# Performance work log

Measured on AMD Instinct MI355X. Metric: run time of the kernel, lower is better.

The kernel has to match this reference:

```python
import jax, jax.numpy as jnp
import numpy as np

N_STATE = 1024
N_HEAD = 16
DIM_PER_HEAD = N_STATE // N_HEAD  # 64
QK_SCALE = DIM_PER_HEAD ** (-0.5)
B, T, T_CACHE = 8, 256, 768


def setup_inputs() -> dict:
    key = jax.random.key(0)
    ks = jax.random.split(key, 12)
    s = 0.02
    return {
        "x": jax.random.normal(ks[0], (B, T, N_STATE), dtype=jnp.float32),
        "qk_mask": jnp.zeros((T, T_CACHE + T), dtype=jnp.float32),
        "cache_k": jax.random.normal(ks[1], (B, T_CACHE, N_STATE), dtype=jnp.float32),
        "cache_v": jax.random.normal(ks[2], (B, T_CACHE, N_STATE), dtype=jnp.float32),
        "Wq": jax.random.normal(ks[3], (N_STATE, N_STATE), dtype=jnp.float32) * s,
        "bq": jax.random.normal(ks[4], (N_STATE,), dtype=jnp.float32) * s,
        "Wk": jax.random.normal(ks[5], (N_STATE, N_STATE), dtype=jnp.float32) * s,
        "Wv": jax.random.normal(ks[6], (N_STATE, N_STATE), dtype=jnp.float32) * s,
        "bv": jax.random.normal(ks[7], (N_STATE,), dtype=jnp.float32) * s,
        "Wo": jax.random.normal(ks[8], (N_STATE, N_STATE), dtype=jnp.float32) * s,
        "bo": jax.random.normal(ks[9], (N_STATE,), dtype=jnp.float32) * s,
    }


def reference(x, qk_mask, cache_k, cache_v, Wq, bq, Wk, Wv, bv, Wo, bo):
    # Linear projections (weights stored as [in, out], i.e. torch weight^T)
    q = (x @ Wq + bq) * QK_SCALE            # [B, T, D]
    new_k = x @ Wk                           # key has no bias
    new_v = x @ Wv + bv
    # KV-cache concat along time
    k = jnp.concatenate([cache_k, new_k], axis=1)  # [B, Tkv, D]
    v = jnp.concatenate([cache_v, new_v], axis=1)
    # Split heads
    Bq, Tq = q.shape[:2]
    Tkv = k.shape[1]
    qh = q.reshape(Bq, Tq, N_HEAD, DIM_PER_HEAD)    # [B, T, H, d]
    kh = k.reshape(Bq, Tkv, N_HEAD, DIM_PER_HEAD)
    vh = v.reshape(Bq, Tkv, N_HEAD, DIM_PER_HEAD)
    # q @ k^T + mask, softmax over keys
    qk = jnp.einsum("bthd,bshd->bhts", qh, kh) + qk_mask  # [B, H, T, Tkv]
    w = jax.nn.softmax(qk, axis=-1).astype(qh.dtype)
    wv = jnp.einsum("bhts,bshd->bthd", w, vh).reshape(Bq, Tq, N_STATE)
    out = wv @ Wo + bo
    return out, new_k, new_v
```

## Files before the change

kernel.cpp:

```cpp
#include <hip/hip_runtime.h>
#include <hip/hip_bf16.h>
#include <stdint.h>

#define Bb 8
#define Tt 256
#define TCC 768
#define TKV 1024
#define NS 1024
#define NH 16
#define DH 64
#define QK_SCALE 0.125f

typedef short bf16x8 __attribute__((ext_vector_type(8)));
typedef float f32x4 __attribute__((ext_vector_type(4)));
typedef unsigned int u32;

__device__ __forceinline__ unsigned short f2bf(float f) {
  union { float f; uint32_t u; } v; v.f = f;
  uint32_t u = v.u;
  u += 0x7fff + ((u >> 16) & 1);
  return (unsigned short)(u >> 16);
}

__device__ __forceinline__ void gload16(const unsigned short* g, unsigned short* l) {
  __builtin_amdgcn_global_load_lds(
      (__attribute__((address_space(1))) u32*)g,
      (__attribute__((address_space(3))) u32*)l,
      16, 0, 0);
}

__global__ __launch_bounds__(256) void prep(
    const float* __restrict__ x, const float* __restrict__ ck,
    const float* __restrict__ Wq, const float* __restrict__ Wk,
    const float* __restrict__ Wv, const float* __restrict__ Wo,
    const float* __restrict__ cv,
    unsigned short* __restrict__ xb, unsigned short* __restrict__ kbw,
    unsigned short* __restrict__ wqt, unsigned short* __restrict__ wkt,
    unsigned short* __restrict__ wvt, unsigned short* __restrict__ wot,
    unsigned short* __restrict__ vbt) {
  __shared__ float tile[64][65];
  int bid = blockIdx.x, tid = threadIdx.x;
  if (bid < 2048) {
    const int64_t nx4 = (int64_t)Bb * Tt * NS / 4;
    const int64_t nk4 = (int64_t)Bb * TCC * NS / 4;
    const int64_t stride = 2048LL * 256;
    for (int64_t t = (int64_t)bid * 256 + tid; t < nx4 + nk4; t += stride) {
      if (t < nx4) {
        float4 v = ((const float4*)x)[t];
        ushort4 o; o.x = f2bf(v.x); o.y = f2bf(v.y); o.z = f2bf(v.z); o.w = f2bf(v.w);
        ((ushort4*)xb)[t] = o;
      } else {
        int64_t e = t - nx4;
        float4 v = ((const float4*)ck)[e];
        ushort4 o; o.x = f2bf(v.x); o.y = f2bf(v.y); o.z = f2bf(v.z); o.w = f2bf(v.w);
        int64_t el = e * 4;
        int64_t b = el / ((int64_t)TCC * NS);
        int64_t rem = el % ((int64_t)TCC * NS);
        int64_t d = b * (int64_t)TKV * NS + rem;
        ((ushort4*)kbw)[d / 4] = o;
      }
    }
    return;
  }
  int tb = bid - 2048;
  const float* src; unsigned short* dst;
  if (tb < 1024) {
    int mat = tb >> 8, t = tb & 255;
    int tr = t >> 4, tc = t & 15;
    const float* W = (mat == 0) ? Wq : (mat == 1) ? Wk : (mat == 2) ? Wv : Wo;
    unsigned short* Wt = (mat == 0) ? wqt : (mat == 1) ? wkt : (mat == 2) ? wvt : wot;
    src = W + (int64_t)(tr * 64) * 1024 + tc * 64;
    dst = Wt + (int64_t)(tc * 64) * 1024 + tr * 64;
  } else {
    int e = tb - 1024;
    int b = e / 192; int t = e % 192;
    int st = t >> 4, ct = t & 15;
    src = cv + (int64_t)b * TCC * NS + (int64_t)(st * 64) * 1024 + ct * 64;
    dst = vbt + (int64_t)b * NS * TKV + (int64_t)(ct * 64) * 1024 + st * 64;
  }
  for (int e = tid; e < 1024; e += 256) {
    int i = e >> 4, j4 = (e & 15) * 4;
    float4 v = *(const float4*)&src[(int64_t)i * 1024 + j4];
    tile[i][j4] = v.x; tile[i][j4 + 1] = v.y; tile[i][j4 + 2] = v.z; tile[i][j4 + 3] = v.w;
  }
  __syncthreads();
  for (int e = tid; e < 1024; e += 256) {
    int i = e >> 4, j4 = (e & 15) * 4;
    ushort4 o;
    o.x = f2bf(tile[j4][i]); o.y = f2bf(tile[j4 + 1][i]);
    o.z = f2bf(tile[j4 + 2][i]); o.w = f2bf(tile[j4 + 3][i]);
    *(ushort4*)&dst[(int64_t)i * 1024 + j4] = o;
  }
}

template <int MODE>
__global__ __launch_bounds__(256) void gemm_mfma(
    const unsigned short* __restrict__ A,
    const unsigned short* __restrict__ Bt0, const unsigned short* __restrict__ Bt1,
    const unsigned short* __restrict__ Bt2,
    const float* __restrict__ bq, const float* __restrict__ bv,
    const float* __restrict__ bo,
    unsigned short* __restrict__ qb,
    float* __restrict__ okf, float* __restrict__ ovf,
    unsigned short* __restrict__ kb, unsigned short* __restrict__ vbt,
    float* __restrict__ outf) {
  constexpr int BM = 64;
  constexpr int BN = (MODE == 0) ? 128 : 64;
  constexpr int MT = 2;
  constexpr int NTf = BN / 32;
  __shared__ __align__(16) unsigned short As[2][BM * 64];
  __shared__ __align__(16) unsigned short Bs[2][BN * 64];

  int tid = threadIdx.x, lane = tid & 63, w = tid >> 6;
  int lr = lane & 15, hi = lane >> 4;
  int wm = w >> 1, wn = w & 1;

  int bid = blockIdx.x;
  int cpx = gridDim.x >> 3;
  int logical = (bid & 7) * cpx + (bid >> 3);

  int tm = logical & 31;
  int tn = logical >> 5;
  int seg, col0;
  const unsigned short* Bt;
  if (MODE == 0) {
    seg = tn >> 3; col0 = (tn & 7) * 128;
    Bt = (seg == 0) ? Bt0 : (seg == 1) ? Bt1 : Bt2;
  } else {
    seg = 0; col0 = tn * 64;
    Bt = Bt0;
  }
  int m0 = tm * 64;

  int srow = lane >> 3;
  int sch8 = (((lane & 7) ^ srow)) * 8;
  int sw = lr & 7;

  f32x4 acc[MT][NTf];
#pragma unroll
  for (int i = 0; i < MT; i++)
#pragma unroll
    for (int j = 0; j < NTf; j++) acc[i][j] = (f32x4){0.f, 0.f, 0.f, 0.f};

  auto STAGE = [&](int buf, int k0) {
#pragma unroll
    for (int i = 0; i < 2; i++) {
      int rb = w * 16 + i * 8;
      gload16(&A[(int64_t)(m0 + rb + srow) * 1024 + k0 + sch8], &As[buf][rb * 64]);
    }
#pragma unroll
    for (int i = 0; i < BN / 32; i++) {
      int rb = w * (BN / 4) + i * 8;
      gload16(&Bt[(int64_t)(col0 + rb + srow) * 1024 + k0 + sch8], &Bs[buf][rb * 64]);
    }
  };

  STAGE(0, 0);
  __syncthreads();
  int cur = 0;
  for (int step = 0; step < 16; ++step) {
    if (step < 15) STAGE(cur ^ 1, (step + 1) * 64);
    bf16x8 af[2][MT], bfr[2][NTf];
#pragma unroll
    for (int kk = 0; kk < 2; kk++) {
      int ch = ((kk * 4 + hi) ^ sw) * 8;
#pragma unroll
      for (int mt = 0; mt < MT; mt++)
        af[kk][mt] = *(const bf16x8*)&As[cur][(wm * 32 + mt * 16 + lr) * 64 + ch];
#pragma unroll
      for (int nt = 0; nt < NTf; nt++)
        bfr[kk][nt] = *(const bf16x8*)&Bs[cur][(wn * (BN / 2) + nt * 16 + lr) * 64 + ch];
    }
#pragma unroll
    for (int kk = 0; kk < 2; kk++)
#pragma unroll
      for (int mt = 0; mt < MT; mt++)
#pragma unroll
        for (int nt = 0; nt < NTf; nt++)
          acc[mt][nt] = __builtin_amdgcn_mfma_f32_16x16x32_bf16(af[kk][mt], bfr[kk][nt],
                                                               acc[mt][nt], 0, 0, 0);
    __syncthreads();
    cur ^= 1;
  }

#pragma unroll
  for (int mt = 0; mt < MT; mt++)
#pragma unroll
    for (int nt = 0; nt < NTf; nt++) {
      int row = m0 + wm * 32 + mt * 16 + hi * 4;
      int col = col0 + wn * (BN / 2) + nt * 16 + lr;
      if (MODE == 1) {
        float bias = bo[col];
#pragma unroll
        for (int r = 0; r < 4; r++)
          outf[(int64_t)(row + r) * 1024 + col] = acc[mt][nt][r] + bias;
      } else if (seg == 0) {
        float bias = bq[col];
#pragma unroll
        for (int r = 0; r < 4; r++)
          qb[(int64_t)(row + r) * 1024 + col] = f2bf((acc[mt][nt][r] + bias) * QK_SCALE);
      } else if (seg == 1) {
#pragma unroll
        for (int r = 0; r < 4; r++) {
          float v = acc[mt][nt][r];
          okf[(int64_t)(row + r) * 1024 + col] = v;
          int b = (row + r) >> 8, t = (row + r) & 255;
          kb[((int64_t)(b * TKV + TCC + t)) * 1024 + col] = f2bf(v);
        }
      } else {
        float bias = bv[col];
        int b = row >> 8, t0 = row & 255;
        int64_t voff = ((int64_t)(b * NH + (col >> 6)) * DH + (col & 63)) * TKV + TCC + t0;
        float v0 = acc[mt][nt][0] + bias, v1 = acc[mt][nt][1] + bias,
              v2 = acc[mt][nt][2] + bias, v3 = acc[mt][nt][3] + bias;
        ovf[(int64_t)(row + 0) * 1024 + col] = v0;
        ovf[(int64_t)(row + 1) * 1024 + col] = v1;
        ovf[(int64_t)(row + 2) * 1024 + col] = v2;
        ovf[(int64_t)(row + 3) * 1024 + col] = v3;
        ushort4 pk; pk.x = f2bf(v0); pk.y = f2bf(v1); pk.z = f2bf(v2); pk.w = f2bf(v3);
        *(ushort4*)&vbt[voff] = pk;
      }
    }
}

__global__ __launch_bounds__(256) void attn(
    const unsigned short* __restrict__ qb, const unsigned short* __restrict__ kb,
    const unsigned short* __restrict__ vbt, const float* __restrict__ mask,
    float* __restrict__ Op, float* __restrict__ Mp, float* __restrict__ Lp) {
  __shared__ __align__(16) unsigned short Ks[2][64 * 64];
  __shared__ __align__(16) unsigned short Vs[2][64 * 64];
  __shared__ unsigned short Ps[4][16 * 76];

  int tid = threadIdx.x, lane = tid & 63, w = tid >> 6;
  int lr = lane & 15, hi = lane >> 4;
  int bid = blockIdx.x;
  int logical = (bid & 7) * 128 + (bid >> 3);
  int s = logical & 1;
  int qt = (logical >> 1) & 3;
  int bh = logical >> 3, b = bh >> 4, h = bh & 15;
  int q0 = qt * 64 + w * 16;
  int kvbase = s * 512;

  const unsigned short* qp = qb + ((int64_t)(b * Tt + q0 + lr)) * 1024 + h * DH + hi * 8;
  bf16x8 aq0 = *(const bf16x8*)qp;
  bf16x8 aq1 = *(const bf16x8*)(qp + 32);

  f32x4 o[4];
#pragma unroll
  for (int nt = 0; nt < 4; nt++) o[nt] = (f32x4){0.f, 0.f, 0.f, 0.f};
  float m[4] = {-1e30f, -1e30f, -1e30f, -1e30f};
  float l[4] = {0.f, 0.f, 0.f, 0.f};

  const unsigned short* kbase = kb + (int64_t)b * TKV * 1024 + h * DH;
  const unsigned short* vbase = vbt + (int64_t)bh * DH * TKV;
  const float* mbase = mask + (int64_t)(q0 + hi * 4) * TKV;

  int srow = lane >> 3;
  int sch8 = ((lane & 7) ^ srow) * 8;
  int sw = lr & 7;

  auto STAGE = [&](int buf, int kv0) {
#pragma unroll
    for (int i = 0; i < 2; i++) {
      int rb = w * 16 + i * 8;
      gload16(&kbase[(int64_t)(kv0 + rb + srow) * 1024 + sch8], &Ks[buf][rb * 64]);
      gload16(&vbase[(int64_t)(rb + srow) * TKV + kv0 + sch8], &Vs[buf][rb * 64]);
    }
  };

  STAGE(0, kvbase);
  __syncthreads();
  int cur = 0;
  for (int c = 0; c < 8; ++c) {
    int kv0 = kvbase + c * 64;
    if (c < 7) STAGE(cur ^ 1, kv0 + 64);

    float mk[4][4];
#pragma unroll
    for (int nt = 0; nt < 4; nt++)
#pragma unroll
      for (int r = 0; r < 4; r++)
        mk[nt][r] = mbase[(int64_t)r * TKV + kv0 + nt * 16 + lr];

    int ch0 = (hi ^ sw) * 8, ch1 = ((hi + 4) ^ sw) * 8;
    f32x4 sc[4];
#pragma unroll
    for (int nt = 0; nt < 4; nt++) {
      int row = (nt * 16 + lr) * 64;
      bf16x8 bk0 = *(const bf16x8*)&Ks[cur][row + ch0];
      bf16x8 bk1 = *(const bf16x8*)&Ks[cur][row + ch1];
      f32x4 z = (f32x4){0.f, 0.f, 0.f, 0.f};
      z = __builtin_amdgcn_mfma_f32_16x16x32_bf16(aq0, bk0, z, 0, 0, 0);
      z = __builtin_amdgcn_mfma_f32_16x16x32_bf16(aq1, bk1, z, 0, 0, 0);
      sc[nt] = z;
    }
#pragma unroll
    for (int nt = 0; nt < 4; nt++)
#pragma unroll
      for (int r = 0; r < 4; r++) sc[nt][r] += mk[nt][r];

    float cm[4];
#pragma unroll
    for (int r = 0; r < 4; r++) {
      cm[r] = fmaxf(fmaxf(sc[0][r], sc[1][r]), fmaxf(sc[2][r], sc[3][r]));
#pragma unroll
      for (int d = 1; d < 16; d <<= 1) cm[r] = fmaxf(cm[r], __shfl_xor(cm[r], d));
    }
#pragma unroll
    for (int r = 0; r < 4; r++) {
      if (cm[r] > m[r] + 8.f) {
        float al = __expf(m[r] - cm[r]);
        m[r] = cm[r];
        l[r] *= al;
        o[0][r] *= al; o[1][r] *= al; o[2][r] *= al; o[3][r] *= al;
      }
    }
    float rs[4] = {0.f, 0.f, 0.f, 0.f};
#pragma unroll
    for (int nt = 0; nt < 4; nt++)
#pragma unroll
      for (int r = 0; r < 4; r++) {
        sc[nt][r] = __expf(sc[nt][r] - m[r]);
        rs[r] += sc[nt][r];
      }
#pragma unroll
    for (int r = 0; r < 4; r++) {
#pragma unroll
      for (int d = 1; d < 16; d <<= 1) rs[r] += __shfl_xor(rs[r], d);
      l[r] += rs[r];
    }

#pragma unroll
    for (int nt = 0; nt < 4; nt++)
#pragma unroll
      for (int r = 0; r < 4; r++)
        Ps[w][(hi * 4 + r) * 76 + nt * 16 + lr] = f2bf(sc[nt][r]);
    bf16x8 pa0 = *(const bf16x8*)&Ps[w][lr * 76 + hi * 8];
    bf16x8 pa1 = *(const bf16x8*)&Ps[w][lr * 76 + 32 + hi * 8];

#pragma unroll
    for (int nt = 0; nt < 4; nt++) {
      int row = (nt * 16 + lr) * 64;
      bf16x8 bv0 = *(const bf16x8*)&Vs[cur][row + ch0];
      bf16x8 bv1 = *(const bf16x8*)&Vs[cur][row + ch1];
      o[nt] = __builtin_amdgcn_mfma_f32_16x16x32_bf16(pa0, bv0, o[nt], 0, 0, 0);
      o[nt] = __builtin_amdgcn_mfma_f32_16x16x32_bf16(pa1, bv1, o[nt], 0, 0, 0);
    }
    __syncthreads();
    cur ^= 1;
  }

  int p = (bh * 4 + qt) * 2 + s;
#pragma unroll
  for (int nt = 0; nt < 4; nt++)
#pragma unroll
    for (int r = 0; r < 4; r++) {
      int row = w * 16 + hi * 4 + r, col = nt * 16 + lr;
      Op[(int64_t)p * 4096 + row * 64 + col] = o[nt][r];
    }
  if (lr == 0) {
#pragma unroll
    for (int r = 0; r < 4; r++) {
      int row = w * 16 + hi * 4 + r;
      Mp[p * 64 + row] = m[r];
      Lp[p * 64 + row] = l[r];
    }
  }
}

__global__ __launch_bounds__(256) void attn_merge(
    const float* __restrict__ Op, const float* __restrict__ Mp,
    const float* __restrict__ Lp, unsigned short* __restrict__ wvb) {
  int t = blockIdx.x * 256 + threadIdx.x;
  int d4 = (t & 15) * 4;
  int row = (t >> 4) & 63;
  int pq = t >> 10;
  int qt = pq & 3, bh = pq >> 2;
  int b = bh >> 4, h = bh & 15;
  int p0 = pq * 2, p1 = p0 + 1;
  float m0 = Mp[p0 * 64 + row], m1 = Mp[p1 * 64 + row];
  float l0 = Lp[p0 * 64 + row], l1 = Lp[p1 * 64 + row];
  float M = fmaxf(m0, m1);
  float w0 = __expf(m0 - M), w1 = __expf(m1 - M);
  float inv = 1.f / (l0 * w0 + l1 * w1);
  float4 o0 = *(const float4*)&Op[((int64_t)p0 * 64 + row) * 64 + d4];
  float4 o1 = *(const float4*)&Op[((int64_t)p1 * 64 + row) * 64 + d4];
  ushort4 pk;
  pk.x = f2bf((o0.x * w0 + o1.x * w1) * inv);
  pk.y = f2bf((o0.y * w0 + o1.y * w1) * inv);
  pk.z = f2bf((o0.z * w0 + o1.z * w1) * inv);
  pk.w = f2bf((o0.w * w0 + o1.w * w1) * inv);
  int q = qt * 64 + row;
  *(ushort4*)&wvb[(int64_t)(b * Tt + q) * 1024 + h * DH + d4] = pk;
}

extern "C" void kernel_launch(void* const* d_in, const int* in_sizes, int n_in,
                              void* d_out, int out_size, void* d_ws, size_t ws_size,
                              hipStream_t stream) {
  const float* x    = (const float*)d_in[0];
  const float* mask = (const float*)d_in[1];
  const float* ck   = (const float*)d_in[2];
  const float* cv   = (const float*)d_in[3];
  const float* Wq   = (const float*)d_in[4];
  const float* bq   = (const float*)d_in[5];
  const float* Wk   = (const float*)d_in[6];
  const float* Wv   = (const float*)d_in[7];
  const float* bv   = (const float*)d_in[8];
  const float* Wo   = (const float*)d_in[9];
  const float* bo   = (const float*)d_in[10];

  const int64_t NT = (int64_t)Bb * Tt * NS;
  float* outp = (float*)d_out;
  float* okf  = outp + NT;
  float* ovf  = outp + 2 * NT;

  char* ws = (char*)d_ws;
  unsigned short* xb  = (unsigned short*)(ws);
  unsigned short* wqt = (unsigned short*)(ws + (4LL << 20));
  unsigned short* wkt = (unsigned short*)(ws + (6LL << 20));
  unsigned short* wvt = (unsigned short*)(ws + (8LL << 20));
  unsigned short* wot = (unsigned short*)(ws + (10LL << 20));
  unsigned short* qbw = (unsigned short*)(ws + (12LL << 20));
  unsigned short* kbw = (unsigned short*)(ws + (16LL << 20));
  unsigned short* vbt = (unsigned short*)(ws + (32LL << 20));
  unsigned short* wvb = (unsigned short*)(ws + (48LL << 20));
  float* Op = (float*)(ws + (52LL << 20));
  float* Mp = (float*)(ws + (68LL << 20));
  float* Lp = (float*)(ws + (69LL << 20));

  prep<<<4608, 256, 0, stream>>>(x, ck, Wq, Wk, Wv, Wo, cv,
                                 xb, kbw, wqt, wkt, wvt, wot, vbt);
  gemm_mfma<0><<<768, 256, 0, stream>>>(xb, wqt, wkt, wvt, bq, bv, bo,
                                        qbw, okf, ovf, kbw, vbt, outp);
  attn<<<1024, 256, 0, stream>>>(qbw, kbw, vbt, mask, Op, Mp, Lp);
  attn_merge<<<2048, 256, 0, stream>>>(Op, Mp, Lp, wvb);
  gemm_mfma<1><<<512, 256, 0, stream>>>(wvb, wot, wot, wot, bq, bv, bo,
                                        qbw, okf, ovf, kbw, vbt, outp);
}
```

Measured before the change: 214.1 us.

## Triple-buffer GEMM and attention loads, drop split-KV attention and merge kernel

Both the GEMM and the attention kernel move from double to triple-buffered LDS staging. Explicit vmcnt waits plus a single barrier per iteration replace the two __syncthreads, so two tiles stay in flight. The attention kernel no longer splits the KV range in two. Each block now walks all 1024 keys and writes the normalized bf16 output directly, which removes the merge kernel and its fp32 partial-result traffic. The cost is half as many attention blocks (512 instead of 1024), so there is less parallelism and each block runs a longer loop, and more LDS is used per block.

```diff
diff --git a/kernel.cpp b/kernel.cpp
--- a/kernel.cpp
+++ b/kernel.cpp
@@ -108,8 +108,8 @@
   constexpr int BN = (MODE == 0) ? 128 : 64;
   constexpr int MT = 2;
   constexpr int NTf = BN / 32;
-  __shared__ __align__(16) unsigned short As[2][BM * 64];
-  __shared__ __align__(16) unsigned short Bs[2][BN * 64];
+  __shared__ __align__(16) unsigned short As[3][BM * 64];
+  __shared__ __align__(16) unsigned short Bs[3][BN * 64];
 
   int tid = threadIdx.x, lane = tid & 63, w = tid >> 6;
   int lr = lane & 15, hi = lane >> 4;
@@ -156,20 +156,30 @@
   };
 
   STAGE(0, 0);
-  __syncthreads();
-  int cur = 0;
+  STAGE(1, 64);
+  int bc = 0;
   for (int step = 0; step < 16; ++step) {
-    if (step < 15) STAGE(cur ^ 1, (step + 1) * 64);
+    if constexpr (MODE == 0) {
+      asm volatile("s_waitcnt vmcnt(6)" ::: "memory");
+    } else {
+      asm volatile("s_waitcnt vmcnt(4)" ::: "memory");
+    }
+    __builtin_amdgcn_s_barrier();
+    __builtin_amdgcn_sched_barrier(0);
+    if (step < 14) {
+      int bs = bc + 2; if (bs >= 3) bs -= 3;
+      STAGE(bs, (step + 2) * 64);
+    }
     bf16x8 af[2][MT], bfr[2][NTf];
 #pragma unroll
     for (int kk = 0; kk < 2; kk++) {
       int ch = ((kk * 4 + hi) ^ sw) * 8;
 #pragma unroll
       for (int mt = 0; mt < MT; mt++)
-        af[kk][mt] = *(const bf16x8*)&As[cur][(wm * 32 + mt * 16 + lr) * 64 + ch];
+        af[kk][mt] = *(const bf16x8*)&As[bc][(wm * 32 + mt * 16 + lr) * 64 + ch];
 #pragma unroll
       for (int nt = 0; nt < NTf; nt++)
-        bfr[kk][nt] = *(const bf16x8*)&Bs[cur][(wn * (BN / 2) + nt * 16 + lr) * 64 + ch];
+        bfr[kk][nt] = *(const bf16x8*)&Bs[bc][(wn * (BN / 2) + nt * 16 + lr) * 64 + ch];
     }
 #pragma unroll
     for (int kk = 0; kk < 2; kk++)
@@ -179,8 +189,7 @@
         for (int nt = 0; nt < NTf; nt++)
           acc[mt][nt] = __builtin_amdgcn_mfma_f32_16x16x32_bf16(af[kk][mt], bfr[kk][nt],
                                                                acc[mt][nt], 0, 0, 0);
-    __syncthreads();
-    cur ^= 1;
+    bc = (bc == 2) ? 0 : bc + 1;
   }
 
 #pragma unroll
@@ -226,20 +235,17 @@
 __global__ __launch_bounds__(256) void attn(
     const unsigned short* __restrict__ qb, const unsigned short* __restrict__ kb,
     const unsigned short* __restrict__ vbt, const float* __restrict__ mask,
-    float* __restrict__ Op, float* __restrict__ Mp, float* __restrict__ Lp) {
-  __shared__ __align__(16) unsigned short Ks[2][64 * 64];
-  __shared__ __align__(16) unsigned short Vs[2][64 * 64];
+    unsigned short* __restrict__ wvb) {
+  __shared__ __align__(16) unsigned short Ks[3][64 * 64];
+  __shared__ __align__(16) unsigned short Vs[3][64 * 64];
   __shared__ unsigned short Ps[4][16 * 76];
 
   int tid = threadIdx.x, lane = tid & 63, w = tid >> 6;
   int lr = lane & 15, hi = lane >> 4;
   int bid = blockIdx.x;
-  int logical = (bid & 7) * 128 + (bid >> 3);
-  int s = logical & 1;
-  int qt = (logical >> 1) & 3;
-  int bh = logical >> 3, b = bh >> 4, h = bh & 15;
+  int logical = (bid & 7) * 64 + (bid >> 3);
+  int qt = logical & 3, bh = logical >> 2, b = bh >> 4, h = bh & 15;
   int q0 = qt * 64 + w * 16;
-  int kvbase = s * 512;
 
   const unsigned short* qp = qb + ((int64_t)(b * Tt + q0 + lr)) * 1024 + h * DH + hi * 8;
   bf16x8 aq0 = *(const bf16x8*)qp;
@@ -268,12 +274,14 @@
     }
   };
 
-  STAGE(0, kvbase);
-  __syncthreads();
-  int cur = 0;
-  for (int c = 0; c < 8; ++c) {
-    int kv0 = kvbase + c * 64;
-    if (c < 7) STAGE(cur ^ 1, kv0 + 64);
+  STAGE(0, 0);
+  STAGE(1, 64);
+  int bc = 0;
+  for (int c = 0; c < 16; ++c) {
+    int kv0 = c * 64;
+    asm volatile("s_waitcnt vmcnt(4)" ::: "memory");
+    __builtin_amdgcn_s_barrier();
+    __builtin_amdgcn_sched_barrier(0);
 
     float mk[4][4];
 #pragma unroll
@@ -282,13 +290,18 @@
       for (int r = 0; r < 4; r++)
         mk[nt][r] = mbase[(int64_t)r * TKV + kv0 + nt * 16 + lr];
 
+    if (c < 14) {
+      int bs = bc + 2; if (bs >= 3) bs -= 3;
+      STAGE(bs, kv0 + 128);
+    }
+
     int ch0 = (hi ^ sw) * 8, ch1 = ((hi + 4) ^ sw) * 8;
     f32x4 sc[4];
 #pragma unroll
     for (int nt = 0; nt < 4; nt++) {
       int row = (nt * 16 + lr) * 64;
-      bf16x8 bk0 = *(const bf16x8*)&Ks[cur][row + ch0];
-      bf16x8 bk1 = *(const bf16x8*)&Ks[cur][row + ch1];
+      bf16x8 bk0 = *(const bf16x8*)&Ks[bc][row + ch0];
+      bf16x8 bk1 = *(const bf16x8*)&Ks[bc][row + ch1];
       f32x4 z = (f32x4){0.f, 0.f, 0.f, 0.f};
       z = __builtin_amdgcn_mfma_f32_16x16x32_bf16(aq0, bk0, z, 0, 0, 0);
       z = __builtin_amdgcn_mfma_f32_16x16x32_bf16(aq1, bk1, z, 0, 0, 0);
@@ -341,57 +354,23 @@
 #pragma unroll
     for (int nt = 0; nt < 4; nt++) {
       int row = (nt * 16 + lr) * 64;
-      bf16x8 bv0 = *(const bf16x8*)&Vs[cur][row + ch0];
-      bf16x8 bv1 = *(const bf16x8*)&Vs[cur][row + ch1];
+      bf16x8 bv0 = *(const bf16x8*)&Vs[bc][row + ch0];
+      bf16x8 bv1 = *(const bf16x8*)&Vs[bc][row + ch1];
       o[nt] = __builtin_amdgcn_mfma_f32_16x16x32_bf16(pa0, bv0, o[nt], 0, 0, 0);
       o[nt] = __builtin_amdgcn_mfma_f32_16x16x32_bf16(pa1, bv1, o[nt], 0, 0, 0);
     }
-    __syncthreads();
-    cur ^= 1;
-  }
-
-  int p = (bh * 4 + qt) * 2 + s;
+    bc = (bc == 2) ? 0 : bc + 1;
+  }
+
+  float inv[4];
+#pragma unroll
+  for (int r = 0; r < 4; r++) inv[r] = 1.f / l[r];
 #pragma unroll
   for (int nt = 0; nt < 4; nt++)
 #pragma unroll
-    for (int r = 0; r < 4; r++) {
-      int row = w * 16 + hi * 4 + r, col = nt * 16 + lr;
-      Op[(int64_t)p * 4096 + row * 64 + col] = o[nt][r];
-    }
-  if (lr == 0) {
-#pragma unroll
-    for (int r = 0; r < 4; r++) {
-      int row = w * 16 + hi * 4 + r;
-      Mp[p * 64 + row] = m[r];
-      Lp[p * 64 + row] = l[r];
-    }
-  }
-}
-
-__global__ __launch_bounds__(256) void attn_merge(
-    const float* __restrict__ Op, const float* __restrict__ Mp,
-    const float* __restrict__ Lp, unsigned short* __restrict__ wvb) {
-  int t = blockIdx.x * 256 + threadIdx.x;
-  int d4 = (t & 15) * 4;
-  int row = (t >> 4) & 63;
-  int pq = t >> 10;
-  int qt = pq & 3, bh = pq >> 2;
-  int b = bh >> 4, h = bh & 15;
-  int p0 = pq * 2, p1 = p0 + 1;
-  float m0 = Mp[p0 * 64 + row], m1 = Mp[p1 * 64 + row];
-  float l0 = Lp[p0 * 64 + row], l1 = Lp[p1 * 64 + row];
-  float M = fmaxf(m0, m1);
-  float w0 = __expf(m0 - M), w1 = __expf(m1 - M);
-  float inv = 1.f / (l0 * w0 + l1 * w1);
-  float4 o0 = *(const float4*)&Op[((int64_t)p0 * 64 + row) * 64 + d4];
-  float4 o1 = *(const float4*)&Op[((int64_t)p1 * 64 + row) * 64 + d4];
-  ushort4 pk;
-  pk.x = f2bf((o0.x * w0 + o1.x * w1) * inv);
-  pk.y = f2bf((o0.y * w0 + o1.y * w1) * inv);
-  pk.z = f2bf((o0.z * w0 + o1.z * w1) * inv);
-  pk.w = f2bf((o0.w * w0 + o1.w * w1) * inv);
-  int q = qt * 64 + row;
-  *(ushort4*)&wvb[(int64_t)(b * Tt + q) * 1024 + h * DH + d4] = pk;
+    for (int r = 0; r < 4; r++)
+      wvb[(int64_t)(b * Tt + q0 + hi * 4 + r) * 1024 + h * DH + nt * 16 + lr] =
+          f2bf(o[nt][r] * inv[r]);
 }
 
 extern "C" void kernel_launch(void* const* d_in, const int* in_sizes, int n_in,
@@ -424,16 +403,12 @@
   unsigned short* kbw = (unsigned short*)(ws + (16LL << 20));
   unsigned short* vbt = (unsigned short*)(ws + (32LL << 20));
   unsigned short* wvb = (unsigned short*)(ws + (48LL << 20));
-  float* Op = (float*)(ws + (52LL << 20));
-  float* Mp = (float*)(ws + (68LL << 20));
-  float* Lp = (float*)(ws + (69LL << 20));
 
   prep<<<4608, 256, 0, stream>>>(x, ck, Wq, Wk, Wv, Wo, cv,
                                  xb, kbw, wqt, wkt, wvt, wot, vbt);
   gemm_mfma<0><<<768, 256, 0, stream>>>(xb, wqt, wkt, wvt, bq, bv, bo,
                                         qbw, okf, ovf, kbw, vbt, outp);
-  attn<<<1024, 256, 0, stream>>>(qbw, kbw, vbt, mask, Op, Mp, Lp);
-  attn_merge<<<2048, 256, 0, stream>>>(Op, Mp, Lp, wvb);
+  attn<<<512, 256, 0, stream>>>(qbw, kbw, vbt, mask, wvb);
   gemm_mfma<1><<<512, 256, 0, stream>>>(wvb, wot, wot, wot, bq, bv, bo,
                                         qbw, okf, ovf, kbw, vbt, outp);
 }
```

New measurement: 211.9 us. No clear change (-1.0%).
